# Optimization experiments

Measured on AMD Instinct MI355X. Metric: run time of the kernel, lower is better.

## Reference

```python
import jax, jax.numpy as jnp
import numpy as np

N = 6144      # number of pedestrians
HID = 256     # hidden_dim
OUT = 32      # out_dim
NTOP = 4      # n nearest neighbours
EMB = OUT // NTOP  # per-neighbour embedding dim = 8


def setup_inputs() -> dict:
    key = jax.random.key(0)
    ks = jax.random.split(key, 12)
    r = lambda k, shp, s=1.0: (jax.random.normal(k, shp, dtype=jnp.float32) * s)
    return {
        "obs1": r(ks[0], (N, 2)),
        "obs2": r(ks[1], (N, 2)),
        "h": r(ks[2], (N, HID), 0.1),
        "c": r(ks[3], (N, HID), 0.1),
        "W_emb": r(ks[4], (4, EMB), 0.3),
        "b_emb": r(ks[5], (EMB,), 0.1),
        "W_ih": r(ks[6], (4 * HID, OUT), 0.1),
        "b_ih": r(ks[7], (4 * HID,), 0.1),
        "W_hh": r(ks[8], (4 * HID, HID), 0.1),
        "b_hh": r(ks[9], (4 * HID,), 0.1),
        "W_pool": r(ks[10], (OUT, HID), 0.1),
        "b_pool": r(ks[11], (OUT,), 0.1),
    }


def reference(obs1, obs2, h, c, W_emb, b_emb, W_ih, b_ih, W_hh, b_hh, W_pool, b_pool):
    n = obs2.shape[0]
    vel = obs2 - obs1                                   # [N,2]
    # rel_position[i, j] = obs2[j] - obs2[i]
    diff = obs2[None, :, :] - obs2[:, None, :]          # [N,N,2]
    dist = jnp.linalg.norm(diff, axis=-1)               # [N,N]
    # exclude self (torch code drops the diagonal before topk)
    dist = jnp.where(jnp.eye(n, dtype=bool), jnp.inf, dist)
    _, idx = jax.lax.top_k(-dist, NTOP)                 # [N,NTOP] indices of nearest
    nearest_pos = jnp.take_along_axis(diff, idx[:, :, None], axis=1)  # [N,NTOP,2]
    # rel_direction[i, j] = vel[j] - vel[i]
    nearest_vel = vel[idx] - vel[:, None, :]            # [N,NTOP,2]
    feat = jnp.concatenate([nearest_pos, nearest_vel], axis=-1)       # [N,NTOP,4]
    # Linear(4, EMB) + ReLU, then flatten neighbours -> [N, OUT]
    emb = jax.nn.relu(feat @ W_emb + b_emb).reshape(n, -1)
    # LSTMCell (PyTorch gate order: i, f, g, o)
    gates = emb @ W_ih.T + b_ih + h @ W_hh.T + b_hh     # [N,4*HID]
    gi, gf, gg, go = jnp.split(gates, 4, axis=-1)
    c_new = jax.nn.sigmoid(gf) * c + jax.nn.sigmoid(gi) * jnp.tanh(gg)
    h_new = jax.nn.sigmoid(go) * jnp.tanh(c_new)
    out = h_new @ W_pool.T + b_pool                     # [N,OUT]
    return out
```

## Files before the change

kernel.cpp:

```cpp
#include <hip/hip_runtime.h>
#include <math.h>

typedef unsigned short u16;
typedef unsigned long long u64;
typedef __attribute__((ext_vector_type(8))) short bf16x8;
typedef __attribute__((ext_vector_type(4))) float f32x4;

__device__ __forceinline__ float sigf(float x)  { return 1.0f / (1.0f + __expf(-x)); }
__device__ __forceinline__ float tanhf_(float x){ float e = __expf(2.0f * x); return 1.0f - 2.0f / (e + 1.0f); }
__device__ __forceinline__ u16 f2bf(float f) {
    unsigned x = __float_as_uint(f);
    return (u16)((x + 0x7fffu + ((x >> 16) & 1u)) >> 16);
}

#define INSU(KEY) do {                                                              \
    u64 _k = (KEY);                                                                 \
    k3 = (_k < k3) ? _k : k3;                                                       \
    { bool _c = k3 < k2; u64 _lo = _c ? k3 : k2, _hi = _c ? k2 : k3; k2 = _lo; k3 = _hi; } \
    { bool _c = k2 < k1; u64 _lo = _c ? k2 : k1, _hi = _c ? k1 : k2; k1 = _lo; k2 = _hi; } \
    { bool _c = k1 < k0; u64 _lo = _c ? k1 : k0, _hi = _c ? k0 : k1; k0 = _lo; k1 = _hi; } \
} while (0)

#define MRG4(X0,X1,X2,X3,Y0,Y1,Y2,Y3) do {                                          \
    float _q0 = fminf((X0),(Y3));                                                   \
    float _q1 = fminf((X1),(Y2));                                                   \
    float _q2 = fminf((X2),(Y1));                                                   \
    float _q3 = fminf((X3),(Y0));                                                   \
    float _l0 = fminf(_q0,_q2), _h0 = fmaxf(_q0,_q2);                               \
    float _l1 = fminf(_q1,_q3), _h1 = fmaxf(_q1,_q3);                               \
    (X0) = fminf(_l0,_l1); (X1) = fmaxf(_l0,_l1);                                   \
    (X2) = fminf(_h0,_h1); (X3) = fmaxf(_h0,_h1);                                   \
} while (0)

#define INS4(D, J) do {                                                              \
    float _d = (D); int _j = (J);                                                    \
    if (_d < bd3 || (_d == bd3 && _j < bj3)) {                                       \
        bd3 = _d; bj3 = _j;                                                          \
        if (bd3 < bd2 || (bd3 == bd2 && bj3 < bj2)) {                                \
            float _t = bd2; bd2 = bd3; bd3 = _t; int _u = bj2; bj2 = bj3; bj3 = _u; }\
        if (bd2 < bd1 || (bd2 == bd1 && bj2 < bj1)) {                                \
            float _t = bd1; bd1 = bd2; bd2 = _t; int _u = bj1; bj1 = bj2; bj2 = _u; }\
        if (bd1 < bd0 || (bd1 == bd0 && bj1 < bj0)) {                                \
            float _t = bd0; bd0 = bd1; bd1 = _t; int _u = bj0; bj0 = bj1; bj1 = _u; }\
    } } while (0)

__global__ void diag_kernel(float* out, int code, int out_size) {
    if (out_size > 0) out[0] = (float)code * 1.0e8f;
}

__device__ __forceinline__ void prep_item(
    int id, const float* Wih, const float* Whh, const float* Wp,
    u16* Wgf, u16* Wpf)
{
    if (id < 36864) {
        int gt = id / 576, rem = id - gt * 576;
        int kt = rem >> 6, ln = rem & 63;
        int g  = gt * 16 + (ln & 15);
        int k  = kt * 32 + (ln >> 4) * 8;
        u16* dst = Wgf + (size_t)id * 8;
        const float* src = (k < 32) ? (Wih + (size_t)g * 32 + k)
                                    : (Whh + (size_t)g * 256 + (k - 32));
        float4 v0 = ((const float4*)src)[0];
        float4 v1 = ((const float4*)src)[1];
        dst[0] = f2bf(v0.x); dst[1] = f2bf(v0.y); dst[2] = f2bf(v0.z); dst[3] = f2bf(v0.w);
        dst[4] = f2bf(v1.x); dst[5] = f2bf(v1.y); dst[6] = f2bf(v1.z); dst[7] = f2bf(v1.w);
    } else if (id < 37888) {
        int id2 = id - 36864;
        int pt = id2 >> 9, rem = id2 & 511;
        int kt = rem >> 6, ln = rem & 63;
        int o  = pt * 16 + (ln & 15);
        int k  = kt * 32 + (ln >> 4) * 8;
        u16* dst = Wpf + (size_t)id2 * 8;
        const float* src = Wp + (size_t)o * 256 + k;
        float4 v0 = ((const float4*)src)[0];
        float4 v1 = ((const float4*)src)[1];
        dst[0] = f2bf(v0.x); dst[1] = f2bf(v0.y); dst[2] = f2bf(v0.z); dst[3] = f2bf(v0.w);
        dst[4] = f2bf(v1.x); dst[5] = f2bf(v1.y); dst[6] = f2bf(v1.z); dst[7] = f2bf(v1.w);
    }
}

__global__ __launch_bounds__(256, 4) void knn_prep_kernel(
    const float* __restrict__ obs1, const float* __restrict__ obs2,
    const float* __restrict__ Wemb, const float* __restrict__ bemb,
    const float* __restrict__ Wih,  const float* __restrict__ Whh,
    const float* __restrict__ Wp,
    u16* __restrict__ Wgf, u16* __restrict__ Wpf,
    int n, int knn_blocks, float* __restrict__ out)
{
    const int t = threadIdx.x;

    if (blockIdx.x >= knn_blocks) {
        int id = (blockIdx.x - knn_blocks) * 256 + t;
        prep_item(id, Wih, Whh, Wp, Wgf, Wpf);
        return;
    }

    const int lane = t & 63;
    const int wv   = t >> 6;
    const int i    = blockIdx.x * 4 + wv;
    if (i >= n) return;

    const float FINF = __int_as_float(0x7f800000);
    const float2* o2 = (const float2*)obs2;
    const float4* o4 = (const float4*)obs2;
    const int n2 = n >> 1;
    const float2 pi = o2[i];

    float mm[8];
    #pragma unroll
    for (int q = 0; q < 8; q++) mm[q] = FINF;

    int f = lane;
    for (; f + 448 < n2; f += 512) {
        float4 p[8];
        #pragma unroll
        for (int q = 0; q < 8; q++) p[q] = o4[f + q * 64];
        #pragma unroll
        for (int q = 0; q < 8; q++) {
            const int j0 = 2 * (f + q * 64);
            float dxa = p[q].x - pi.x, dya = p[q].y - pi.y;
            float da = __fadd_rn(__fmul_rn(dxa, dxa), __fmul_rn(dya, dya));
            da = (j0 == i) ? FINF : da;
            float dxb = p[q].z - pi.x, dyb = p[q].w - pi.y;
            float db = __fadd_rn(__fmul_rn(dxb, dxb), __fmul_rn(dyb, dyb));
            db = (j0 + 1 == i) ? FINF : db;
            mm[q] = fminf(mm[q], fminf(da, db));
        }
    }
    for (; f < n2; f += 64) {
        float4 p = o4[f];
        const int j0 = 2 * f;
        float dxa = p.x - pi.x, dya = p.y - pi.y;
        float da = __fadd_rn(__fmul_rn(dxa, dxa), __fmul_rn(dya, dya));
        da = (j0 == i) ? FINF : da;
        float dxb = p.z - pi.x, dyb = p.w - pi.y;
        float db = __fadd_rn(__fmul_rn(dxb, dxb), __fmul_rn(dyb, dyb));
        db = (j0 + 1 == i) ? FINF : db;
        mm[0] = fminf(mm[0], fminf(da, db));
    }
    if ((n & 1) && lane == 0) {
        float2 pj = o2[n - 1];
        float dx = pj.x - pi.x, dy = pj.y - pi.y;
        float d2 = __fadd_rn(__fmul_rn(dx, dx), __fmul_rn(dy, dy));
        d2 = (n - 1 == i) ? FINF : d2;
        mm[1] = fminf(mm[1], d2);
    }
    const float mn = fminf(fminf(fminf(mm[0], mm[1]), fminf(mm[2], mm[3])),
                           fminf(fminf(mm[4], mm[5]), fminf(mm[6], mm[7])));

    float A0 = mn, A1 = FINF, A2 = FINF, A3 = FINF;
    #pragma unroll
    for (int m = 1; m < 64; m <<= 1) {
        float y0 = __shfl_xor(A0, m), y1 = __shfl_xor(A1, m);
        float y2 = __shfl_xor(A2, m), y3 = __shfl_xor(A3, m);
        MRG4(A0, A1, A2, A3, y0, y1, y2, y3);
    }
    const float thr = A3;

    u64 k0 = ~0ull, k1 = ~0ull, k2 = ~0ull, k3 = ~0ull;

    f = lane;
    for (; f + 448 < n2; f += 512) {
        float4 p[8];
        #pragma unroll
        for (int q = 0; q < 8; q++) p[q] = o4[f + q * 64];
        #pragma unroll
        for (int q = 0; q < 8; q++) {
            const int j0 = 2 * (f + q * 64);
            float dxa = p[q].x - pi.x, dya = p[q].y - pi.y;
            float da = __fadd_rn(__fmul_rn(dxa, dxa), __fmul_rn(dya, dya));
            if (da <= thr) {
                u64 key = (((u64)__float_as_uint(da)) << 24) | (unsigned)j0;
                key = (j0 == i) ? ~0ull : key;
                INSU(key);
            }
            float dxb = p[q].z - pi.x, dyb = p[q].w - pi.y;
            float db = __fadd_rn(__fmul_rn(dxb, dxb), __fmul_rn(dyb, dyb));
            if (db <= thr) {
                u64 key = (((u64)__float_as_uint(db)) << 24) | (unsigned)(j0 + 1);
                key = (j0 + 1 == i) ? ~0ull : key;
                INSU(key);
            }
        }
    }
    for (; f < n2; f += 64) {
        float4 p = o4[f];
        const int j0 = 2 * f;
        float dxa = p.x - pi.x, dya = p.y - pi.y;
        float da = __fadd_rn(__fmul_rn(dxa, dxa), __fmul_rn(dya, dya));
        if (da <= thr) {
            u64 key = (((u64)__float_as_uint(da)) << 24) | (unsigned)j0;
            key = (j0 == i) ? ~0ull : key;
            INSU(key);
        }
        float dxb = p.z - pi.x, dyb = p.w - pi.y;
        float db = __fadd_rn(__fmul_rn(dxb, dxb), __fmul_rn(dyb, dyb));
        if (db <= thr) {
            u64 key = (((u64)__float_as_uint(db)) << 24) | (unsigned)(j0 + 1);
            key = (j0 + 1 == i) ? ~0ull : key;
            INSU(key);
        }
    }
    if ((n & 1) && lane == 0) {
        float2 pj = o2[n - 1];
        float dx = pj.x - pi.x, dy = pj.y - pi.y;
        float d2 = __fadd_rn(__fmul_rn(dx, dx), __fmul_rn(dy, dy));
        if (d2 <= thr) {
            u64 key = (((u64)__float_as_uint(d2)) << 24) | (unsigned)(n - 1);
            key = (n - 1 == i) ? ~0ull : key;
            INSU(key);
        }
    }

    #pragma unroll
    for (int m = 1; m < 64; m <<= 1) {
        u64 o0 = __shfl_xor(k0, m), o1 = __shfl_xor(k1, m);
        u64 o2_ = __shfl_xor(k2, m), o3 = __shfl_xor(k3, m);
        INSU(o0); INSU(o1); INSU(o2_); INSU(o3);
    }

    if (lane < 4) {
        u64 kq = (lane == 0) ? k0 : (lane == 1) ? k1 : (lane == 2) ? k2 : k3;
        int jn = (int)(kq & 0xFFFFFF);
        if (jn < 0 || jn >= n) jn = 0;
        float pix = pi.x, piy = pi.y;
        float pjx = obs2[2 * jn], pjy = obs2[2 * jn + 1];
        float px = pjx - pix, py = pjy - piy;
        float vix = pix - obs1[2 * i];
        float viy = piy - obs1[2 * i + 1];
        float vx = (pjx - obs1[2 * jn])     - vix;
        float vy = (pjy - obs1[2 * jn + 1]) - viy;
        float* dst = out + (size_t)i * 32 + lane * 8;
        #pragma unroll
        for (int e = 0; e < 8; e++) {
            float a = px * Wemb[e]      + py * Wemb[8 + e]
                    + vx * Wemb[16 + e] + vy * Wemb[24 + e]
                    + bemb[e];
            dst[e] = fmaxf(a, 0.0f);
        }
    }
}

__global__ __launch_bounds__(512) void lstm_kernel(
    const float* __restrict__ h,   const float* __restrict__ c,
    const u16*  __restrict__ Wgf,  const float* __restrict__ bih,
    const float* __restrict__ bhh,
    const u16*  __restrict__ Wpf,  const float* __restrict__ bp,
    int n, float* __restrict__ out)
{
    __shared__ __align__(16) char lds[17920];
    u16* sXb = (u16*)lds;
    u16* sHb = (u16*)(lds + 9472);

    const int t    = threadIdx.x;
    const int i0   = blockIdx.x * 12;
    const int lane = t & 63;
    const int wv   = t >> 6;
    const int fm   = lane & 15;
    const int fq   = lane >> 4;

    {
        int r = t >> 5, e = t & 31;
        int row = i0 + r;
        float v = (r < 12 && row < n) ? out[(size_t)row * 32 + e] : 0.0f;
        sXb[r * 296 + e] = f2bf(v);
    }
    #pragma unroll
    for (int f = t; f < 16 * 64; f += 512) {
        int r = f >> 6, k4 = f & 63;
        int row = i0 + r;
        float4 hv = (r < 12 && row < n) ? ((const float4*)h)[(size_t)row * 64 + k4]
                                        : make_float4(0.f, 0.f, 0.f, 0.f);
        u16* d = &sXb[r * 296 + 32 + k4 * 4];
        d[0] = f2bf(hv.x); d[1] = f2bf(hv.y); d[2] = f2bf(hv.z); d[3] = f2bf(hv.w);
    }
    __syncthreads();

    bf16x8 afr[9];
    #pragma unroll
    for (int kt = 0; kt < 9; kt++)
        afr[kt] = *(const bf16x8*)&sXb[fm * 296 + kt * 32 + fq * 8];

    #pragma unroll
    for (int ut2 = 0; ut2 < 2; ut2++) {
        const int ut = wv + ut2 * 8;
        const int u  = ut * 16 + fm;

        f32x4 acc[4];
        #pragma unroll
        for (int jg = 0; jg < 4; jg++) acc[jg] = (f32x4){0.f, 0.f, 0.f, 0.f};

        #pragma unroll
        for (int jg = 0; jg < 4; jg++) {
            const int gt = jg * 16 + ut;
            const u16* wbase = Wgf + ((size_t)gt * 9) * 512 + lane * 8;
            #pragma unroll
            for (int kt = 0; kt < 9; kt++) {
                bf16x8 bfr = *(const bf16x8*)(wbase + kt * 512);
                acc[jg] = __builtin_amdgcn_mfma_f32_16x16x32_bf16(afr[kt], bfr, acc[jg], 0, 0, 0);
            }
        }

        float b0 = bih[u]       + bhh[u];
        float b1 = bih[u + 256] + bhh[u + 256];
        float b2 = bih[u + 512] + bhh[u + 512];
        float b3 = bih[u + 768] + bhh[u + 768];

        #pragma unroll
        for (int r_ = 0; r_ < 4; r_++) {
            int rl = fq * 4 + r_;
            int row = i0 + rl;
            bool valid = (rl < 12) && (row < n);
            float cin = valid ? c[(size_t)row * 256 + u] : 0.0f;
            float gi = acc[0][r_] + b0;
            float gf = acc[1][r_] + b1;
            float gg = acc[2][r_] + b2;
            float go = acc[3][r_] + b3;
            float cn = sigf(gf) * cin + sigf(gi) * tanhf_(gg);
            float hn = sigf(go) * tanhf_(cn);
            sHb[rl * 264 + u] = valid ? f2bf(hn) : (u16)0;
        }
    }
    __syncthreads();

    if (wv < 2) {
        bf16x8 ah[8];
        #pragma unroll
        for (int kt = 0; kt < 8; kt++)
            ah[kt] = *(const bf16x8*)&sHb[fm * 264 + kt * 32 + fq * 8];
        const u16* wbase = Wpf + ((size_t)wv * 8) * 512 + lane * 8;
        f32x4 acc = {0.f, 0.f, 0.f, 0.f};
        #pragma unroll
        for (int kt = 0; kt < 8; kt++) {
            bf16x8 bfr = *(const bf16x8*)(wbase + kt * 512);
            acc = __builtin_amdgcn_mfma_f32_16x16x32_bf16(ah[kt], bfr, acc, 0, 0, 0);
        }
        float bias = bp[wv * 16 + fm];
        #pragma unroll
        for (int r_ = 0; r_ < 4; r_++) {
            int rl = fq * 4 + r_;
            int row = i0 + rl;
            if (rl < 12 && row < n) out[(size_t)row * 32 + wv * 16 + fm] = acc[r_] + bias;
        }
    }
}

__global__ __launch_bounds__(256) void nnlstm_fallback(
    const float* __restrict__ obs1, const float* __restrict__ obs2,
    const float* __restrict__ h,    const float* __restrict__ c,
    const float* __restrict__ Wemb, const float* __restrict__ bemb,
    const float* __restrict__ Wih,  const float* __restrict__ bih,
    const float* __restrict__ Whh,  const float* __restrict__ bhh,
    const float* __restrict__ Wp,   const float* __restrict__ bp,
    int n, float* __restrict__ out)
{
    __shared__ float sMd[16][64];
    __shared__ int   sMj[16][64];
    __shared__ float sX[16][292];
    __shared__ float sH[16][264];

    const int t   = threadIdx.x;
    const int sub = t & 15;
    const int ii  = t >> 4;
    const int i0  = blockIdx.x * 16;
    const int i   = i0 + ii;

    for (int v = t; v < 16 * 256; v += 256) {
        int r = v >> 8, k = v & 255;
        int row = i0 + r;
        sX[r][32 + k] = (row < n) ? h[(size_t)row * 256 + k] : 0.0f;
    }

    float bd0 = 1e30f, bd1 = 1e30f, bd2 = 1e30f, bd3 = 1e30f;
    int   bj0 = 0x7fffffff, bj1 = 0x7fffffff, bj2 = 0x7fffffff, bj3 = 0x7fffffff;

    if (i < n) {
        const float pix = obs2[2 * i];
        const float piy = obs2[2 * i + 1];
        for (int j = sub; j < n; j += 16) {
            float dx = obs2[2 * j]     - pix;
            float dy = obs2[2 * j + 1] - piy;
            float d2 = __fadd_rn(__fmul_rn(dx, dx), __fmul_rn(dy, dy));
            float dist = __fsqrt_rn(d2);
            if (j == i) continue;
            INS4(dist, j);
        }
    }
    sMd[ii][sub * 4 + 0] = bd0;  sMj[ii][sub * 4 + 0] = bj0;
    sMd[ii][sub * 4 + 1] = bd1;  sMj[ii][sub * 4 + 1] = bj1;
    sMd[ii][sub * 4 + 2] = bd2;  sMj[ii][sub * 4 + 2] = bj2;
    sMd[ii][sub * 4 + 3] = bd3;  sMj[ii][sub * 4 + 3] = bj3;
    __syncthreads();

    if (t < 16) {
        const int r = t;
        const int irow = i0 + r;
        float bd0 = 1e30f, bd1 = 1e30f, bd2 = 1e30f, bd3 = 1e30f;
        int   bj0 = 0x7fffffff, bj1 = 0x7fffffff, bj2 = 0x7fffffff, bj3 = 0x7fffffff;
        for (int q = 0; q < 64; q++) { INS4(sMd[r][q], sMj[r][q]); }

        if (irow < n) {
            float pix = obs2[2 * irow], piy = obs2[2 * irow + 1];
            float vix = pix - obs1[2 * irow];
            float viy = piy - obs1[2 * irow + 1];
            #pragma unroll
            for (int q2 = 0; q2 < 4; q2++) {
                int jn = (q2 == 0) ? bj0 : (q2 == 1) ? bj1 : (q2 == 2) ? bj2 : bj3;
                if (jn < 0 || jn >= n) jn = 0;
                float pjx = obs2[2 * jn], pjy = obs2[2 * jn + 1];
                float px = pjx - pix, py = pjy - piy;
                float vx = (pjx - obs1[2 * jn])     - vix;
                float vy = (pjy - obs1[2 * jn + 1]) - viy;
                #pragma unroll
                for (int e = 0; e < 8; e++) {
                    float a = px * Wemb[e]      + py * Wemb[8 + e]
                            + vx * Wemb[16 + e] + vy * Wemb[24 + e]
                            + bemb[e];
                    sX[r][q2 * 8 + e] = fmaxf(a, 0.0f);
                }
            }
        } else {
            for (int e = 0; e < 32; e++) sX[r][e] = 0.0f;
        }
    }
    __syncthreads();

    const int uu = t;
    float acc[4][16];
    #pragma unroll
    for (int j = 0; j < 4; j++) {
        float b = bih[uu + 256 * j] + bhh[uu + 256 * j];
        #pragma unroll
        for (int r = 0; r < 16; r++) acc[j][r] = b;
    }

    for (int kc = 0; kc < 288; kc++) {
        float w[4];
        #pragma unroll
        for (int j = 0; j < 4; j++) {
            int g = uu + 256 * j;
            w[j] = (kc < 32) ? Wih[(size_t)g * 32 + kc]
                             : Whh[(size_t)g * 256 + (kc - 32)];
        }
        #pragma unroll
        for (int r = 0; r < 16; r++) {
            float x = sX[r][kc];
            #pragma unroll
            for (int j = 0; j < 4; j++) acc[j][r] += w[j] * x;
        }
    }

    for (int r = 0; r < 16; r++) {
        int row = i0 + r;
        float cin = (row < n) ? c[(size_t)row * 256 + uu] : 0.0f;
        float cn = sigf(acc[1][r]) * cin + sigf(acc[0][r]) * tanhf(acc[2][r]);
        float hn = sigf(acc[3][r]) * tanhf(cn);
        sH[r][uu] = hn;
    }
    __syncthreads();

    for (int v = t; v < 16 * 32; v += 256) {
        int r = v >> 5, o = v & 31;
        int row = i0 + r;
        if (row >= n) continue;
        float a = bp[o];
        for (int kc = 0; kc < 256; kc++)
            a += Wp[(size_t)o * 256 + kc] * sH[r][kc];
        out[(size_t)row * 32 + o] = a;
    }
}

extern "C" void kernel_launch(void* const* d_in, const int* in_sizes, int n_in,
                              void* d_out, int out_size, void* d_ws, size_t ws_size,
                              hipStream_t stream) {
    float* out = (float*)d_out;

    int code = 0, n = 0;
    if (n_in != 12) code = 1;
    else {
        n = in_sizes[1] / 2;
        if (n <= 4 || in_sizes[1] != 2 * n)          code = 2;
        else if (in_sizes[0]  != 2 * n)              code = 3;
        else if (in_sizes[2]  != 256 * n)            code = 4;
        else if (in_sizes[3]  != 256 * n)            code = 5;
        else if (in_sizes[4]  != 32 || in_sizes[5] != 8)        code = 6;
        else if (in_sizes[6]  != 32768 || in_sizes[7] != 1024)  code = 7;
        else if (in_sizes[8]  != 262144 || in_sizes[9] != 1024) code = 8;
        else if (in_sizes[10] != 8192 || in_sizes[11] != 32)    code = 9;
        else if (out_size != 32 * n)                 code = 10;
    }
    if (code != 0) {
        diag_kernel<<<1, 1, 0, stream>>>(out, code, out_size);
        return;
    }

    const float* obs1   = (const float*)d_in[0];
    const float* obs2   = (const float*)d_in[1];
    const float* h      = (const float*)d_in[2];
    const float* c      = (const float*)d_in[3];
    const float* W_emb  = (const float*)d_in[4];
    const float* b_emb  = (const float*)d_in[5];
    const float* W_ih   = (const float*)d_in[6];
    const float* b_ih   = (const float*)d_in[7];
    const float* W_hh   = (const float*)d_in[8];
    const float* b_hh   = (const float*)d_in[9];
    const float* W_pool = (const float*)d_in[10];
    const float* b_pool = (const float*)d_in[11];

    const size_t wgf_bytes = (size_t)36864 * 8 * sizeof(u16);
    const size_t wpf_bytes = (size_t)1024 * 8 * sizeof(u16);

    if (ws_size >= wgf_bytes + wpf_bytes && n <= (1 << 24)) {
        u16* Wgf = (u16*)d_ws;
        u16* Wpf = (u16*)((char*)d_ws + wgf_bytes);
        int knn_blocks = (n + 3) / 4;
        knn_prep_kernel<<<knn_blocks + 148, 256, 0, stream>>>(
            obs1, obs2, W_emb, b_emb, W_ih, W_hh, W_pool, Wgf, Wpf,
            n, knn_blocks, out);
        lstm_kernel<<<(n + 11) / 12, 512, 0, stream>>>(
            h, c, Wgf, b_ih, b_hh, Wpf, b_pool, n, out);
    } else {
        nnlstm_fallback<<<(n + 15) / 16, 256, 0, stream>>>(
            obs1, obs2, h, c, W_emb, b_emb, W_ih, b_ih, W_hh, b_hh,
            W_pool, b_pool, n, out);
    }
}
```

Baseline: 133.8 us.

## Stage obs2 positions in LDS for KNN search with 512-thread blocks

Adds a KNN kernel that copies all obs2 positions into shared memory once per 512-thread block (8 query rows per block). Both the min-threshold pass and the selection pass then read from LDS instead of global/L2. For N=6144 the copy is 48KB, which limits occupancy, and every block repeats the full copy. The old global kernel is kept as a fallback for larger n, with its 8-way unrolled selection loop removed.

```diff
diff --git a/kernel.cpp b/kernel.cpp
--- a/kernel.cpp
+++ b/kernel.cpp
@@ -79,6 +79,154 @@
     }
 }
 
+__global__ __launch_bounds__(512, 6) void knn_prep_lds_kernel(
+    const float* __restrict__ obs1, const float* __restrict__ obs2,
+    const float* __restrict__ Wemb, const float* __restrict__ bemb,
+    const float* __restrict__ Wih,  const float* __restrict__ Whh,
+    const float* __restrict__ Wp,
+    u16* __restrict__ Wgf, u16* __restrict__ Wpf,
+    int n, int knn_blocks, float* __restrict__ out)
+{
+    extern __shared__ __align__(16) char smem[];
+    float4* s4 = (float4*)smem;
+    float2* sP = (float2*)smem;
+
+    const int t = threadIdx.x;
+
+    if (blockIdx.x >= knn_blocks) {
+        int id = (blockIdx.x - knn_blocks) * 512 + t;
+        prep_item(id, Wih, Whh, Wp, Wgf, Wpf);
+        return;
+    }
+
+    const float FINF = __int_as_float(0x7f800000);
+    const float2* o2 = (const float2*)obs2;
+    const float4* o4 = (const float4*)obs2;
+    const int n2 = n >> 1;
+
+    for (int idx = t; idx < n2; idx += 512) s4[idx] = o4[idx];
+    if ((n & 1) && t == 0) sP[n - 1] = o2[n - 1];
+    __syncthreads();
+
+    const int lane = t & 63;
+    const int wv   = t >> 6;
+    const int i    = blockIdx.x * 8 + wv;
+    if (i >= n) return;
+
+    const float2 pi = o2[i];
+
+    float mm0 = FINF, mm1 = FINF, mm2 = FINF, mm3 = FINF;
+
+    int f = lane;
+    for (; f + 64 < n2; f += 128) {
+        float4 pa = s4[f], pb = s4[f + 64];
+        int j0 = 2 * f;
+        float dxa = pa.x - pi.x, dya = pa.y - pi.y;
+        float da = __fadd_rn(__fmul_rn(dxa, dxa), __fmul_rn(dya, dya));
+        da = (j0 == i) ? FINF : da;
+        float dxb = pa.z - pi.x, dyb = pa.w - pi.y;
+        float db = __fadd_rn(__fmul_rn(dxb, dxb), __fmul_rn(dyb, dyb));
+        db = (j0 + 1 == i) ? FINF : db;
+        mm0 = fminf(mm0, da); mm1 = fminf(mm1, db);
+        int j1 = 2 * (f + 64);
+        float dxc = pb.x - pi.x, dyc = pb.y - pi.y;
+        float dc = __fadd_rn(__fmul_rn(dxc, dxc), __fmul_rn(dyc, dyc));
+        dc = (j1 == i) ? FINF : dc;
+        float dxd = pb.z - pi.x, dyd = pb.w - pi.y;
+        float dd = __fadd_rn(__fmul_rn(dxd, dxd), __fmul_rn(dyd, dyd));
+        dd = (j1 + 1 == i) ? FINF : dd;
+        mm2 = fminf(mm2, dc); mm3 = fminf(mm3, dd);
+    }
+    for (; f < n2; f += 64) {
+        float4 pa = s4[f];
+        int j0 = 2 * f;
+        float dxa = pa.x - pi.x, dya = pa.y - pi.y;
+        float da = __fadd_rn(__fmul_rn(dxa, dxa), __fmul_rn(dya, dya));
+        da = (j0 == i) ? FINF : da;
+        float dxb = pa.z - pi.x, dyb = pa.w - pi.y;
+        float db = __fadd_rn(__fmul_rn(dxb, dxb), __fmul_rn(dyb, dyb));
+        db = (j0 + 1 == i) ? FINF : db;
+        mm0 = fminf(mm0, da); mm1 = fminf(mm1, db);
+    }
+    if ((n & 1) && lane == 0) {
+        float2 pj = sP[n - 1];
+        float dx = pj.x - pi.x, dy = pj.y - pi.y;
+        float d2 = __fadd_rn(__fmul_rn(dx, dx), __fmul_rn(dy, dy));
+        d2 = (n - 1 == i) ? FINF : d2;
+        mm2 = fminf(mm2, d2);
+    }
+    const float mn = fminf(fminf(mm0, mm1), fminf(mm2, mm3));
+
+    float A0 = mn, A1 = FINF, A2 = FINF, A3 = FINF;
+    #pragma unroll
+    for (int m = 1; m < 64; m <<= 1) {
+        float y0 = __shfl_xor(A0, m), y1 = __shfl_xor(A1, m);
+        float y2 = __shfl_xor(A2, m), y3 = __shfl_xor(A3, m);
+        MRG4(A0, A1, A2, A3, y0, y1, y2, y3);
+    }
+    const float thr = A3;
+
+    u64 k0 = ~0ull, k1 = ~0ull, k2 = ~0ull, k3 = ~0ull;
+
+    f = lane;
+    for (; f < n2; f += 64) {
+        float4 pa = s4[f];
+        const int j0 = 2 * f;
+        float dxa = pa.x - pi.x, dya = pa.y - pi.y;
+        float da = __fadd_rn(__fmul_rn(dxa, dxa), __fmul_rn(dya, dya));
+        if (da <= thr) {
+            u64 key = (((u64)__float_as_uint(da)) << 24) | (unsigned)j0;
+            key = (j0 == i) ? ~0ull : key;
+            INSU(key);
+        }
+        float dxb = pa.z - pi.x, dyb = pa.w - pi.y;
+        float db = __fadd_rn(__fmul_rn(dxb, dxb), __fmul_rn(dyb, dyb));
+        if (db <= thr) {
+            u64 key = (((u64)__float_as_uint(db)) << 24) | (unsigned)(j0 + 1);
+            key = (j0 + 1 == i) ? ~0ull : key;
+            INSU(key);
+        }
+    }
+    if ((n & 1) && lane == 0) {
+        float2 pj = sP[n - 1];
+        float dx = pj.x - pi.x, dy = pj.y - pi.y;
+        float d2 = __fadd_rn(__fmul_rn(dx, dx), __fmul_rn(dy, dy));
+        if (d2 <= thr) {
+            u64 key = (((u64)__float_as_uint(d2)) << 24) | (unsigned)(n - 1);
+            key = (n - 1 == i) ? ~0ull : key;
+            INSU(key);
+        }
+    }
+
+    #pragma unroll
+    for (int m = 1; m < 64; m <<= 1) {
+        u64 o0 = __shfl_xor(k0, m), o1 = __shfl_xor(k1, m);
+        u64 o2_ = __shfl_xor(k2, m), o3 = __shfl_xor(k3, m);
+        INSU(o0); INSU(o1); INSU(o2_); INSU(o3);
+    }
+
+    if (lane < 4) {
+        u64 kq = (lane == 0) ? k0 : (lane == 1) ? k1 : (lane == 2) ? k2 : k3;
+        int jn = (int)(kq & 0xFFFFFF);
+        if (jn < 0 || jn >= n) jn = 0;
+        float pix = pi.x, piy = pi.y;
+        float pjx = obs2[2 * jn], pjy = obs2[2 * jn + 1];
+        float px = pjx - pix, py = pjy - piy;
+        float vix = pix - obs1[2 * i];
+        float viy = piy - obs1[2 * i + 1];
+        float vx = (pjx - obs1[2 * jn])     - vix;
+        float vy = (pjy - obs1[2 * jn + 1]) - viy;
+        float* dst = out + (size_t)i * 32 + lane * 8;
+        #pragma unroll
+        for (int e = 0; e < 8; e++) {
+            float a = px * Wemb[e]      + py * Wemb[8 + e]
+                    + vx * Wemb[16 + e] + vy * Wemb[24 + e]
+                    + bemb[e];
+            dst[e] = fmaxf(a, 0.0f);
+        }
+    }
+}
+
 __global__ __launch_bounds__(256, 4) void knn_prep_kernel(
     const float* __restrict__ obs1, const float* __restrict__ obs2,
     const float* __restrict__ Wemb, const float* __restrict__ bemb,
@@ -160,29 +308,6 @@
     u64 k0 = ~0ull, k1 = ~0ull, k2 = ~0ull, k3 = ~0ull;
 
     f = lane;
-    for (; f + 448 < n2; f += 512) {
-        float4 p[8];
-        #pragma unroll
-        for (int q = 0; q < 8; q++) p[q] = o4[f + q * 64];
-        #pragma unroll
-        for (int q = 0; q < 8; q++) {
-            const int j0 = 2 * (f + q * 64);
-            float dxa = p[q].x - pi.x, dya = p[q].y - pi.y;
-            float da = __fadd_rn(__fmul_rn(dxa, dxa), __fmul_rn(dya, dya));
-            if (da <= thr) {
-                u64 key = (((u64)__float_as_uint(da)) << 24) | (unsigned)j0;
-                key = (j0 == i) ? ~0ull : key;
-                INSU(key);
-            }
-            float dxb = p[q].z - pi.x, dyb = p[q].w - pi.y;
-            float db = __fadd_rn(__fmul_rn(dxb, dxb), __fmul_rn(dyb, dyb));
-            if (db <= thr) {
-                u64 key = (((u64)__float_as_uint(db)) << 24) | (unsigned)(j0 + 1);
-                key = (j0 + 1 == i) ? ~0ull : key;
-                INSU(key);
-            }
-        }
-    }
     for (; f < n2; f += 64) {
         float4 p = o4[f];
         const int j0 = 2 * f;
@@ -513,10 +638,19 @@
     if (ws_size >= wgf_bytes + wpf_bytes && n <= (1 << 24)) {
         u16* Wgf = (u16*)d_ws;
         u16* Wpf = (u16*)((char*)d_ws + wgf_bytes);
-        int knn_blocks = (n + 3) / 4;
-        knn_prep_kernel<<<knn_blocks + 148, 256, 0, stream>>>(
-            obs1, obs2, W_emb, b_emb, W_ih, W_hh, W_pool, Wgf, Wpf,
-            n, knn_blocks, out);
+        const size_t lds_bytes = (size_t)((n + 1) & ~1) * 8;
+        if (lds_bytes <= 49152) {
+            int knn_blocks = (n + 7) / 8;
+            int prep_blocks = (37888 + 511) / 512;
+            knn_prep_lds_kernel<<<knn_blocks + prep_blocks, 512, lds_bytes, stream>>>(
+                obs1, obs2, W_emb, b_emb, W_ih, W_hh, W_pool, Wgf, Wpf,
+                n, knn_blocks, out);
+        } else {
+            int knn_blocks = (n + 3) / 4;
+            knn_prep_kernel<<<knn_blocks + 148, 256, 0, stream>>>(
+                obs1, obs2, W_emb, b_emb, W_ih, W_hh, W_pool, Wgf, Wpf,
+                n, knn_blocks, out);
+        }
         lstm_kernel<<<(n + 11) / 12, 512, 0, stream>>>(
             h, c, Wgf, b_ih, b_hh, Wpf, b_pool, n, out);
     } else {
```

Result: faster. 131.1 us (-2.1%).
